# Performance work log

Hardware: AMD Instinct MI355X
Metric: run time of the kernel (lower is better)

## Reference

```python
import jax, jax.numpy as jnp
import numpy as np

KERNEL = 7  # neighborhood window (7x7)
NUM_HEADS = 4


def _window_idx(L, k):
    # NATTEN edge-clamped window start: each query attends to exactly k neighbors.
    starts = jnp.clip(jnp.arange(L) - k // 2, 0, L - k)  # [L]
    return starts[:, None] + jnp.arange(k)[None, :]       # [L, k]


def setup_inputs() -> dict:
    key = jax.random.key(0)
    k1, k2, k3, k4, k5 = jax.random.split(key, 5)
    B, H, W, D = 8, 64, 64, 128
    return {
        "x": jax.random.normal(k1, (B, H, W, D), dtype=jnp.float32),
        "w_qkv": jax.random.normal(k2, (3 * D, D), dtype=jnp.float32) * 0.02,
        "b_qkv": jax.random.normal(k3, (3 * D,), dtype=jnp.float32) * 0.02,
        "w_proj": jax.random.normal(k4, (D, D), dtype=jnp.float32) * 0.02,
        "b_proj": jax.random.normal(k5, (D,), dtype=jnp.float32) * 0.02,
    }


def reference(x, w_qkv, b_qkv, w_proj, b_proj):
    B, H, W, D = x.shape
    nh, k = NUM_HEADS, KERNEL
    hd = D // nh
    scale = hd ** -0.5

    # QKV projection -> [3, B, nh, H, W, hd]
    qkv = x @ w_qkv.T + b_qkv
    qkv = qkv.reshape(B, H, W, 3, nh, hd).transpose(3, 0, 4, 1, 2, 5)
    q, kk, v = qkv[0], qkv[1], qkv[2]

    idx_h = _window_idx(H, k)  # [H, k]
    idx_w = _window_idx(W, k)  # [W, k]
    IH = idx_h[:, None, :, None]  # [H,1,k,1]
    IW = idx_w[None, :, None, :]  # [1,W,1,k]

    # Gather local K/V neighborhoods: [B, nh, H, W, k, k, hd] -> [B, nh, H, W, k*k, hd]
    kn = kk[:, :, IH, IW, :].reshape(B, nh, H, W, k * k, hd)
    vn = v[:, :, IH, IW, :].reshape(B, nh, H, W, k * k, hd)

    attn = jnp.einsum('bhxyd,bhxynd->bhxyn', q * scale, kn)
    attn = jax.nn.softmax(attn, axis=-1)
    out = jnp.einsum('bhxyn,bhxynd->bhxyd', attn, vn)

    out = out.transpose(0, 2, 3, 1, 4).reshape(B, H, W, D)
    return out @ w_proj.T + b_proj
```

## Files before the change

### kernel.cpp

```cpp
#include <hip/hip_runtime.h>
#include <hip/hip_bf16.h>

#define BB 8
#define HH 64
#define WW 64
#define DD 128
#define NH 4
#define HD 32
#define KS 7
#define TS 8
#define HALO 14

typedef __attribute__((ext_vector_type(8))) short short8v;
typedef __attribute__((ext_vector_type(4))) short short4v;
typedef __attribute__((ext_vector_type(4))) float f32x4;
typedef unsigned short bf16_t;

__device__ inline short f2bf(float f) {
  union { float f; unsigned u; } x; x.f = f;
  unsigned r = x.u + 0x7FFFu + ((x.u >> 16) & 1u);
  return (short)(r >> 16);
}

__global__ __launch_bounds__(256) void qkv_mfma(
    const float* __restrict__ x, const float* __restrict__ w,
    const float* __restrict__ bqkv,
    bf16_t* __restrict__ q, bf16_t* __restrict__ k, bf16_t* __restrict__ v) {
  __shared__ __align__(16) short smA[128 * 128];
  __shared__ __align__(16) short smB[128 * 128];
  const int tid = threadIdx.x;
  const int m_tile = blockIdx.x;
  const int n_tile = blockIdx.y;

  const float* Ab = x + (size_t)m_tile * 128 * 128;
  const float* Bb = w + (size_t)n_tile * 128 * 128;
#pragma unroll
  for (int i = 0; i < 8; i++) {
    int idx = tid + i * 256;
    int r = idx >> 4, p = idx & 15;
    const float* ap = Ab + r * 128 + p * 8;
    float4 a0 = *(const float4*)ap;
    float4 a1 = *(const float4*)(ap + 4);
    short8v s;
    s[0] = f2bf(a0.x); s[1] = f2bf(a0.y); s[2] = f2bf(a0.z); s[3] = f2bf(a0.w);
    s[4] = f2bf(a1.x); s[5] = f2bf(a1.y); s[6] = f2bf(a1.z); s[7] = f2bf(a1.w);
    *(short8v*)((char*)smA + ((r * 256 + p * 16) ^ ((r & 7) << 4))) = s;
    const float* bp_ = Bb + r * 128 + p * 8;
    float4 b0 = *(const float4*)bp_;
    float4 b1 = *(const float4*)(bp_ + 4);
    short8v t;
    t[0] = f2bf(b0.x); t[1] = f2bf(b0.y); t[2] = f2bf(b0.z); t[3] = f2bf(b0.w);
    t[4] = f2bf(b1.x); t[5] = f2bf(b1.y); t[6] = f2bf(b1.z); t[7] = f2bf(b1.w);
    *(short8v*)((char*)smB + ((r * 256 + p * 16) ^ ((r & 7) << 4))) = t;
  }
  __syncthreads();

  const int lane = tid & 63;
  const int wid = tid >> 6;
  const int wm = wid >> 1, wn = wid & 1;
  const int l15 = lane & 15, l4 = lane >> 4;

  f32x4 acc[4][4] = {};
  const int rowA0 = wm * 64 + l15;
  const int rowB0 = wn * 64 + l15;
  const int swzA = (rowA0 & 7) << 4;
  const int swzB = (rowB0 & 7) << 4;

#pragma unroll
  for (int ks = 0; ks < 4; ks++) {
    const int cb = ks * 64 + l4 * 16;
    short8v a[4], b[4];
#pragma unroll
    for (int i = 0; i < 4; i++) {
      a[i] = *(const short8v*)((const char*)smA + ((((rowA0 + i * 16) * 256) + cb) ^ swzA));
      b[i] = *(const short8v*)((const char*)smB + ((((rowB0 + i * 16) * 256) + cb) ^ swzB));
    }
#pragma unroll
    for (int mi = 0; mi < 4; mi++)
#pragma unroll
      for (int nj = 0; nj < 4; nj++)
        acc[mi][nj] = __builtin_amdgcn_mfma_f32_16x16x32_bf16(a[mi], b[nj], acc[mi][nj], 0, 0, 0);
  }

  __syncthreads();
  short* smC = smA;
  const float qscale = 0.17677669529663687f;
#pragma unroll
  for (int nj = 0; nj < 4; nj++) {
    const int n_local = wn * 64 + nj * 16 + l15;
    const int n = n_tile * 128 + n_local;
    const float bias = bqkv[n];
    const float sc = (n_tile == 0) ? qscale : 1.f;
#pragma unroll
    for (int mi = 0; mi < 4; mi++) {
#pragma unroll
      for (int r = 0; r < 4; r++) {
        const int m = wm * 64 + mi * 16 + l4 * 4 + r;
        *(bf16_t*)((char*)smC + ((m * 256 + n_local * 2) ^ ((m & 7) << 4))) =
            (bf16_t)f2bf((acc[mi][nj][r] + bias) * sc);
      }
    }
  }
  __syncthreads();

  const int bblk = m_tile >> 5;
  bf16_t* outp = (n_tile == 0) ? q : ((n_tile == 1) ? k : v);
#pragma unroll
  for (int i = 0; i < 8; i++) {
    const int idx = i * 256 + tid;
    const int h = idx >> 9;
    const int rem = idx & 511;
    const int m = rem >> 2, c = rem & 3;
    short8v t8 = *(const short8v*)((const char*)smC +
        ((m * 256 + h * 64 + c * 16) ^ ((m & 7) << 4)));
    const int pix = (m_tile * 128 + m) & 4095;
    *(short8v*)(outp + ((size_t)(bblk * 4 + h)) * 131072 + (size_t)pix * 32 + c * 8) = t8;
  }
}

__global__ __launch_bounds__(256) void attn_mfma(
    const bf16_t* __restrict__ q, const bf16_t* __restrict__ k,
    const bf16_t* __restrict__ v, bf16_t* __restrict__ ao) {
  __shared__ __align__(16) char lds[14336 + 16384];
  char* ksb = lds;
  char* vtb = lds + 14336;

  const int tile = blockIdx.x;
  const int tx = tile >> 3, ty = tile & 7;
  const int head = blockIdx.y, bb = blockIdx.z;
  const size_t bh = ((size_t)bb * NH + head) * 4096;
  const bf16_t* kb = k + bh * HD;
  const bf16_t* vb = v + bh * HD;
  const bf16_t* qb = q + bh * HD;
  const int rstart = min(max(tx * TS - 3, 0), HH - HALO);
  const int cstart = min(max(ty * TS - 3, 0), WW - HALO);
  const int tid = threadIdx.x;
  const int lane = tid & 63, wid = tid >> 6;
  const int l15 = lane & 15, h = lane >> 4;

  short8v qf;
  int qx, qy;
  {
    const int pit = wid * 16 + l15;
    qx = tx * TS + (pit >> 3);
    qy = ty * TS + (pit & 7);
    qf = *(const short8v*)(qb + ((size_t)(qx * WW + qy)) * HD + h * 8);
  }
  const int wx0 = min(max(qx - 3, 0), HH - KS) - rstart;
  const int wy0 = min(max(qy - 3, 0), WW - KS) - cstart;

  const int x0 = tx * TS + wid * 2;
  const int w0 = min(max(x0 - 3, 0), HH - KS) - rstart;
  const int base = min(w0 & ~1, 4);

  for (int idx = tid; idx < 784; idx += 256) {
    const int p = idx >> 2, f = idx & 3;
    const int pr = p / HALO, pc = p % HALO;
    const size_t g = ((size_t)((rstart + pr) * WW + (cstart + pc))) * HD + f * 8;
    short8v kv8 = *(const short8v*)(kb + g);
    const int slot = pr * 16 + pc;
    *(short8v*)(ksb + ((slot * 64 + f * 16) ^ (((slot >> 1) & 3) << 4))) = kv8;
  }
  for (int idx = tid; idx < 784; idx += 256) {
    const int pp = idx >> 3, c = idx & 7;
    const int pr = pp / 7, pc2 = (pp % 7) * 2;
    const size_t g = ((size_t)((rstart + pr) * WW + (cstart + pc2))) * HD + c * 4;
    short4v v0 = *(const short4v*)(vb + g);
    short4v v1 = *(const short4v*)(vb + g + HD);
    const int pos0 = ((pr >> 1) << 5) + ((pc2 >> 2) << 3) + ((pr & 1) << 2) + (pc2 & 3);
#pragma unroll
    for (int j = 0; j < 4; j++) {
      const int d = c * 4 + j;
      const unsigned pk2 = (unsigned)(unsigned short)v0[j] |
                           ((unsigned)(unsigned short)v1[j] << 16);
      *(unsigned*)(vtb + ((d * 512 + pos0 * 2) ^ ((d & 7) << 4))) = pk2;
    }
  }
  for (int idx = tid; idx < 512; idx += 256) {
    const int d = idx >> 4, pr = idx & 15;
    if (pr < 14) {
      const int pos = ((pr >> 1) << 5) + 24 + ((pr & 1) << 2) + 2;
      *(unsigned*)(vtb + ((d * 512 + pos * 2) ^ ((d & 7) << 4))) = 0u;
    }
  }
  __syncthreads();

  f32x4 acc[10];
  const f32x4 zf = {0.f, 0.f, 0.f, 0.f};
  __builtin_amdgcn_s_setprio(1);
#pragma unroll
  for (int nt = 0; nt < 10; nt++) {
    const int slot = (base + nt) * 16 + l15;
    short8v kf = *(const short8v*)(ksb + ((slot * 64 + h * 16) ^ (((slot >> 1) & 3) << 4)));
    acc[nt] = __builtin_amdgcn_mfma_f32_16x16x32_bf16(kf, qf, zf, 0, 0, 0);
  }
  __builtin_amdgcn_s_setprio(0);

  bool cv[4];
#pragma unroll
  for (int r = 0; r < 4; r++) cv[r] = ((unsigned)(h * 4 + r - wy0) < 7u);
  float sum = 0.f;
#pragma unroll
  for (int nt = 0; nt < 10; nt++) {
    const bool rv = ((unsigned)(base + nt - wx0) < 7u);
#pragma unroll
    for (int r = 0; r < 4; r++) {
      const float p = (rv && cv[r]) ? __expf(acc[nt][r]) : 0.f;
      acc[nt][r] = p;
      sum += p;
    }
  }
  sum += __shfl_xor(sum, 16);
  sum += __shfl_xor(sum, 32);
  const float inv = 1.f / sum;

  unsigned pk[10][2];
#pragma unroll
  for (int nt = 0; nt < 10; nt++) {
    pk[nt][0] = (unsigned)(unsigned short)f2bf(acc[nt][0] * inv) |
                ((unsigned)(unsigned short)f2bf(acc[nt][1] * inv) << 16);
    pk[nt][1] = (unsigned)(unsigned short)f2bf(acc[nt][2] * inv) |
                ((unsigned)(unsigned short)f2bf(acc[nt][3] * inv) << 16);
  }

  f32x4 o0 = zf, o1 = zf;
  const int swzv = (l15 & 7) << 4;
  const int cbase = (base >> 1) * 64;
  __builtin_amdgcn_s_setprio(1);
#pragma unroll
  for (int kc = 0; kc < 5; kc++) {
    union { unsigned u[4]; short8v s; } pa;
    pa.u[0] = pk[2 * kc][0];     pa.u[1] = pk[2 * kc][1];
    pa.u[2] = pk[2 * kc + 1][0]; pa.u[3] = pk[2 * kc + 1][1];
    const int boff = cbase + kc * 64 + h * 16;
    short8v vb0 = *(const short8v*)(vtb + ((l15 * 512 + boff) ^ swzv));
    short8v vb1 = *(const short8v*)(vtb + (((l15 + 16) * 512 + boff) ^ swzv));
    o0 = __builtin_amdgcn_mfma_f32_16x16x32_bf16(pa.s, vb0, o0, 0, 0, 0);
    o1 = __builtin_amdgcn_mfma_f32_16x16x32_bf16(pa.s, vb1, o1, 0, 0, 0);
  }
  __builtin_amdgcn_s_setprio(0);

#pragma unroll
  for (int r = 0; r < 4; r++) {
    const int pit = wid * 16 + h * 4 + r;
    const int x = tx * TS + (pit >> 3), y = ty * TS + (pit & 7);
    bf16_t* op = ao + ((size_t)bb * 4096 + x * WW + y) * DD + head * HD;
    op[l15]      = (bf16_t)f2bf(o0[r]);
    op[l15 + 16] = (bf16_t)f2bf(o1[r]);
  }
}

__global__ __launch_bounds__(256) void proj_mfma(
    const bf16_t* __restrict__ aob, const float* __restrict__ wp,
    const float* __restrict__ bp, float* __restrict__ out) {
  __shared__ __align__(16) char plds[65536];
  short* smA = (short*)plds;
  short* smB = (short*)(plds + 32768);
  const int tid = threadIdx.x;
  const int m_tile = blockIdx.x;

  const bf16_t* Ab = aob + (size_t)m_tile * 128 * 128;
#pragma unroll
  for (int i = 0; i < 8; i++) {
    int idx = tid + i * 256;
    int r = idx >> 4, p = idx & 15;
    short8v s = *(const short8v*)(Ab + r * 128 + p * 8);
    *(short8v*)((char*)smA + ((r * 256 + p * 16) ^ ((r & 7) << 4))) = s;
    const float* bp_ = wp + r * 128 + p * 8;
    float4 b0 = *(const float4*)bp_;
    float4 b1 = *(const float4*)(bp_ + 4);
    short8v t;
    t[0] = f2bf(b0.x); t[1] = f2bf(b0.y); t[2] = f2bf(b0.z); t[3] = f2bf(b0.w);
    t[4] = f2bf(b1.x); t[5] = f2bf(b1.y); t[6] = f2bf(b1.z); t[7] = f2bf(b1.w);
    *(short8v*)((char*)smB + ((r * 256 + p * 16) ^ ((r & 7) << 4))) = t;
  }
  __syncthreads();

  const int lane = tid & 63;
  const int wid = tid >> 6;
  const int wm = wid >> 1, wn = wid & 1;
  const int l15 = lane & 15, l4 = lane >> 4;

  f32x4 acc[4][4] = {};
  const int rowA0 = wm * 64 + l15;
  const int rowB0 = wn * 64 + l15;
  const int swzA = (rowA0 & 7) << 4;
  const int swzB = (rowB0 & 7) << 4;

#pragma unroll
  for (int ks = 0; ks < 4; ks++) {
    const int cb = ks * 64 + l4 * 16;
    short8v a[4], b[4];
#pragma unroll
    for (int i = 0; i < 4; i++) {
      a[i] = *(const short8v*)((const char*)smA + ((((rowA0 + i * 16) * 256) + cb) ^ swzA));
      b[i] = *(const short8v*)((const char*)smB + ((((rowB0 + i * 16) * 256) + cb) ^ swzB));
    }
#pragma unroll
    for (int mi = 0; mi < 4; mi++)
#pragma unroll
      for (int nj = 0; nj < 4; nj++)
        acc[mi][nj] = __builtin_amdgcn_mfma_f32_16x16x32_bf16(a[mi], b[nj], acc[mi][nj], 0, 0, 0);
  }

  __syncthreads();
#pragma unroll
  for (int nj = 0; nj < 4; nj++) {
    const int n = wn * 64 + nj * 16 + l15;
    const float bias = bp[n];
#pragma unroll
    for (int mi = 0; mi < 4; mi++) {
#pragma unroll
      for (int r = 0; r < 4; r++) {
        const int m = wm * 64 + mi * 16 + l4 * 4 + r;
        *(float*)(plds + ((m * 512 + n * 4) ^ ((m & 7) << 5))) = acc[mi][nj][r] + bias;
      }
    }
  }
  __syncthreads();

#pragma unroll
  for (int i = 0; i < 16; i++) {
    const int idx = i * 256 + tid;
    const int m = idx >> 5, c = idx & 31;
    float4 t = *(const float4*)(plds + ((m * 512 + c * 16) ^ ((m & 7) << 5)));
    *(float4*)(out + (size_t)(m_tile * 128 + m) * DD + c * 4) = t;
  }
}

extern "C" void kernel_launch(void* const* d_in, const int* in_sizes, int n_in,
                              void* d_out, int out_size, void* d_ws, size_t ws_size,
                              hipStream_t stream) {
  const float* x      = (const float*)d_in[0];
  const float* w_qkv  = (const float*)d_in[1];
  const float* b_qkv  = (const float*)d_in[2];
  const float* w_proj = (const float*)d_in[3];
  const float* b_proj = (const float*)d_in[4];
  float* out = (float*)d_out;

  const size_t per = (size_t)BB * NH * HH * WW * HD;
  bf16_t* q  = (bf16_t*)d_ws;
  bf16_t* k  = q + per;
  bf16_t* v  = k + per;
  bf16_t* ao = v + per;

  qkv_mfma<<<dim3(256, 3), dim3(256), 0, stream>>>(x, w_qkv, b_qkv, q, k, v);
  attn_mfma<<<dim3(64, NH, BB), dim3(256), 0, stream>>>(q, k, v, ao);
  proj_mfma<<<dim3(256), dim3(256), 0, stream>>>(ao, w_proj, b_proj, out);
}
```

Measured before the change: 46.13 us.

## Load K fragments directly from global, overlap V staging with QK MFMAs

The K halo is no longer staged in LDS. Each lane loads its K fragments straight from global memory, with the column clamped to 13, and the QK MFMAs are issued before the V transpose store and the barrier. V global loads are issued first into registers so their latency overlaps the QK compute. LDS use drops to the V buffer only, which may improve occupancy. In exchange K is re-read redundantly from global and L2, since neighbouring waves share rows and lanes 14 and 15 duplicate column 13.

```diff
diff --git a/kernel.cpp b/kernel.cpp
--- a/kernel.cpp
+++ b/kernel.cpp
@@ -121,9 +121,7 @@
 __global__ __launch_bounds__(256) void attn_mfma(
     const bf16_t* __restrict__ q, const bf16_t* __restrict__ k,
     const bf16_t* __restrict__ v, bf16_t* __restrict__ ao) {
-  __shared__ __align__(16) char lds[14336 + 16384];
-  char* ksb = lds;
-  char* vtb = lds + 14336;
+  __shared__ __align__(16) char vtb[16384];
 
   const int tile = blockIdx.x;
   const int tx = tile >> 3, ty = tile & 7;
@@ -136,7 +134,7 @@
   const int cstart = min(max(ty * TS - 3, 0), WW - HALO);
   const int tid = threadIdx.x;
   const int lane = tid & 63, wid = tid >> 6;
-  const int l15 = lane & 15, h = lane >> 4;
+  const int l15 = lane & 15, h4 = lane >> 4;
 
   short8v qf;
   int qx, qy;
@@ -144,7 +142,7 @@
     const int pit = wid * 16 + l15;
     qx = tx * TS + (pit >> 3);
     qy = ty * TS + (pit & 7);
-    qf = *(const short8v*)(qb + ((size_t)(qx * WW + qy)) * HD + h * 8);
+    qf = *(const short8v*)(qb + ((size_t)(qx * WW + qy)) * HD + h4 * 8);
   }
   const int wx0 = min(max(qx - 3, 0), HH - KS) - rstart;
   const int wy0 = min(max(qy - 3, 0), WW - KS) - cstart;
@@ -153,27 +151,51 @@
   const int w0 = min(max(x0 - 3, 0), HH - KS) - rstart;
   const int base = min(w0 & ~1, 4);
 
-  for (int idx = tid; idx < 784; idx += 256) {
-    const int p = idx >> 2, f = idx & 3;
-    const int pr = p / HALO, pc = p % HALO;
-    const size_t g = ((size_t)((rstart + pr) * WW + (cstart + pc))) * HD + f * 8;
-    short8v kv8 = *(const short8v*)(kb + g);
-    const int slot = pr * 16 + pc;
-    *(short8v*)(ksb + ((slot * 64 + f * 16) ^ (((slot >> 1) & 3) << 4))) = kv8;
-  }
-  for (int idx = tid; idx < 784; idx += 256) {
-    const int pp = idx >> 3, c = idx & 7;
-    const int pr = pp / 7, pc2 = (pp % 7) * 2;
-    const size_t g = ((size_t)((rstart + pr) * WW + (cstart + pc2))) * HD + c * 4;
-    short4v v0 = *(const short4v*)(vb + g);
-    short4v v1 = *(const short4v*)(vb + g + HD);
-    const int pos0 = ((pr >> 1) << 5) + ((pc2 >> 2) << 3) + ((pr & 1) << 2) + (pc2 & 3);
-#pragma unroll
-    for (int j = 0; j < 4; j++) {
-      const int d = c * 4 + j;
-      const unsigned pk2 = (unsigned)(unsigned short)v0[j] |
-                           ((unsigned)(unsigned short)v1[j] << 16);
-      *(unsigned*)(vtb + ((d * 512 + pos0 * 2) ^ ((d & 7) << 4))) = pk2;
+  short4v vl[4][2];
+#pragma unroll
+  for (int t = 0; t < 4; t++) {
+    const int idx = tid + t * 256;
+    if (idx < 784) {
+      const int pp = idx >> 3, c = idx & 7;
+      const int pr = pp / 7, pc2 = (pp % 7) * 2;
+      const size_t g = ((size_t)((rstart + pr) * WW + (cstart + pc2))) * HD + c * 4;
+      vl[t][0] = *(const short4v*)(vb + g);
+      vl[t][1] = *(const short4v*)(vb + g + HD);
+    }
+  }
+
+  f32x4 acc[10];
+  const f32x4 zf = {0.f, 0.f, 0.f, 0.f};
+  const int kcol = cstart + min(l15, 13);
+#pragma unroll
+  for (int ch = 0; ch < 2; ch++) {
+    short8v kf[5];
+#pragma unroll
+    for (int i = 0; i < 5; i++) {
+      const int pr = rstart + base + ch * 5 + i;
+      kf[i] = *(const short8v*)(kb + ((size_t)(pr * WW + kcol)) * HD + h4 * 8);
+    }
+    __builtin_amdgcn_s_setprio(1);
+#pragma unroll
+    for (int i = 0; i < 5; i++)
+      acc[ch * 5 + i] = __builtin_amdgcn_mfma_f32_16x16x32_bf16(kf[i], qf, zf, 0, 0, 0);
+    __builtin_amdgcn_s_setprio(0);
+  }
+
+#pragma unroll
+  for (int t = 0; t < 4; t++) {
+    const int idx = tid + t * 256;
+    if (idx < 784) {
+      const int pp = idx >> 3, c = idx & 7;
+      const int pr = pp / 7, pc2 = (pp % 7) * 2;
+      const int pos0 = ((pr >> 1) << 5) + ((pc2 >> 2) << 3) + ((pr & 1) << 2) + (pc2 & 3);
+#pragma unroll
+      for (int j = 0; j < 4; j++) {
+        const int d = c * 4 + j;
+        const unsigned pk2 = (unsigned)(unsigned short)vl[t][0][j] |
+                             ((unsigned)(unsigned short)vl[t][1][j] << 16);
+        *(unsigned*)(vtb + ((d * 512 + pos0 * 2) ^ ((d & 7) << 4))) = pk2;
+      }
     }
   }
   for (int idx = tid; idx < 512; idx += 256) {
@@ -185,20 +207,9 @@
   }
   __syncthreads();
 
-  f32x4 acc[10];
-  const f32x4 zf = {0.f, 0.f, 0.f, 0.f};
-  __builtin_amdgcn_s_setprio(1);
-#pragma unroll
-  for (int nt = 0; nt < 10; nt++) {
-    const int slot = (base + nt) * 16 + l15;
-    short8v kf = *(const short8v*)(ksb + ((slot * 64 + h * 16) ^ (((slot >> 1) & 3) << 4)));
-    acc[nt] = __builtin_amdgcn_mfma_f32_16x16x32_bf16(kf, qf, zf, 0, 0, 0);
-  }
-  __builtin_amdgcn_s_setprio(0);
-
   bool cv[4];
 #pragma unroll
-  for (int r = 0; r < 4; r++) cv[r] = ((unsigned)(h * 4 + r - wy0) < 7u);
+  for (int r = 0; r < 4; r++) cv[r] = ((unsigned)(h4 * 4 + r - wy0) < 7u);
   float sum = 0.f;
 #pragma unroll
   for (int nt = 0; nt < 10; nt++) {
@@ -214,15 +225,6 @@
   sum += __shfl_xor(sum, 32);
   const float inv = 1.f / sum;
 
-  unsigned pk[10][2];
-#pragma unroll
-  for (int nt = 0; nt < 10; nt++) {
-    pk[nt][0] = (unsigned)(unsigned short)f2bf(acc[nt][0] * inv) |
-                ((unsigned)(unsigned short)f2bf(acc[nt][1] * inv) << 16);
-    pk[nt][1] = (unsigned)(unsigned short)f2bf(acc[nt][2] * inv) |
-                ((unsigned)(unsigned short)f2bf(acc[nt][3] * inv) << 16);
-  }
-
   f32x4 o0 = zf, o1 = zf;
   const int swzv = (l15 & 7) << 4;
   const int cbase = (base >> 1) * 64;
@@ -230,9 +232,15 @@
 #pragma unroll
   for (int kc = 0; kc < 5; kc++) {
     union { unsigned u[4]; short8v s; } pa;
-    pa.u[0] = pk[2 * kc][0];     pa.u[1] = pk[2 * kc][1];
-    pa.u[2] = pk[2 * kc + 1][0]; pa.u[3] = pk[2 * kc + 1][1];
-    const int boff = cbase + kc * 64 + h * 16;
+    pa.u[0] = (unsigned)(unsigned short)f2bf(acc[2 * kc][0] * inv) |
+              ((unsigned)(unsigned short)f2bf(acc[2 * kc][1] * inv) << 16);
+    pa.u[1] = (unsigned)(unsigned short)f2bf(acc[2 * kc][2] * inv) |
+              ((unsigned)(unsigned short)f2bf(acc[2 * kc][3] * inv) << 16);
+    pa.u[2] = (unsigned)(unsigned short)f2bf(acc[2 * kc + 1][0] * inv) |
+              ((unsigned)(unsigned short)f2bf(acc[2 * kc + 1][1] * inv) << 16);
+    pa.u[3] = (unsigned)(unsigned short)f2bf(acc[2 * kc + 1][2] * inv) |
+              ((unsigned)(unsigned short)f2bf(acc[2 * kc + 1][3] * inv) << 16);
+    const int boff = cbase + kc * 64 + h4 * 16;
     short8v vb0 = *(const short8v*)(vtb + ((l15 * 512 + boff) ^ swzv));
     short8v vb1 = *(const short8v*)(vtb + (((l15 + 16) * 512 + boff) ^ swzv));
     o0 = __builtin_amdgcn_mfma_f32_16x16x32_bf16(pa.s, vb0, o0, 0, 0, 0);
@@ -242,7 +250,7 @@
 
 #pragma unroll
   for (int r = 0; r < 4; r++) {
-    const int pit = wid * 16 + h * 4 + r;
+    const int pit = wid * 16 + h4 * 4 + r;
     const int x = tx * TS + (pit >> 3), y = ty * TS + (pit & 7);
     bf16_t* op = ao + ((size_t)bb * 4096 + x * WW + y) * DD + head * HD;
     op[l15]      = (bf16_t)f2bf(o0[r]);
```

New measurement: 44.45 us. -3.6%, faster.
